# Kernel optimization log

Measured on AMD Instinct MI355X. Metric: run time of the kernel, lower is better.

Reference implementation:

```python
import jax, jax.numpy as jnp
import numpy as np
from jax import lax

B, F_BINS, T = 4, 196, 1000
DM, H, DEPTH, FFN, L, EDIM = 512, 8, 64, 2048, 4, 128


def setup_inputs() -> dict:
    key = jax.random.key(0)
    ks = jax.random.split(key, 16)
    d = {}
    d['spec'] = jax.random.normal(ks[0], (B, 1, F_BINS, T), jnp.float32)
    d['conv1_w'] = jax.random.normal(ks[1], (32, 1, 5, 5), jnp.float32) / 5.0
    d['conv1_b'] = jax.random.normal(ks[2], (32,), jnp.float32) * 0.01
    d['conv2_w'] = jax.random.normal(ks[3], (64, 32, 5, 5), jnp.float32) / np.sqrt(32 * 25)
    d['conv2_b'] = jax.random.normal(ks[4], (64,), jnp.float32) * 0.01
    d['proj_w'] = jax.random.normal(ks[5], (DM, 64), jnp.float32) / 8.0
    d['proj_b'] = jnp.zeros((DM,), jnp.float32)
    d['ln1_g'] = jnp.ones((L, DM), jnp.float32)
    d['ln1_b'] = jnp.zeros((L, DM), jnp.float32)
    s = 1.0 / np.sqrt(DM)
    for i, nm in enumerate(['qw', 'kw', 'vw', 'dw']):
        d[nm] = jax.random.normal(ks[6 + i], (L, DM, DM), jnp.float32) * s
    for nm in ['qb', 'kb', 'vb', 'db']:
        d[nm] = jnp.zeros((L, DM), jnp.float32)
    d['Er'] = jax.random.normal(ks[10], (L, T, DEPTH), jnp.float32)
    d['ln2_g'] = jnp.ones((L, DM), jnp.float32)
    d['ln2_b'] = jnp.zeros((L, DM), jnp.float32)
    d['f1w'] = jax.random.normal(ks[11], (L, FFN, DM), jnp.float32) * s
    d['f1b'] = jnp.zeros((L, FFN), jnp.float32)
    d['f2w'] = jax.random.normal(ks[12], (L, DM, FFN), jnp.float32) / np.sqrt(FFN)
    d['f2b'] = jnp.zeros((L, DM), jnp.float32)
    d['deproj_w'] = jax.random.normal(ks[13], (EDIM, DM), jnp.float32) * s
    d['deproj_b'] = jnp.zeros((EDIM,), jnp.float32)
    return d


def _layernorm(x, g, b, eps=1e-5):
    mu = jnp.mean(x, -1, keepdims=True)
    var = jnp.mean(jnp.square(x - mu), -1, keepdims=True)
    return g * (x - mu) / jnp.sqrt(var + eps) + b


def _skew(QEr):
    # QEr: [B,H,S,S] -> music-transformer skew trick
    b, h, s, _ = QEr.shape
    padded = jnp.pad(QEr, ((0, 0), (0, 0), (0, 0), (1, 0)))  # [B,H,S,S+1]
    return padded.reshape(b, h, s + 1, s)[:, :, 1:, :]


def _forward(spec, conv1_w, conv1_b, conv2_w, conv2_b, proj_w, proj_b,
             ln1_g, ln1_b, qw, qb, kw, kb, vw, vb, dw, db, Er,
             ln2_g, ln2_b, f1w, f1b, f2w, f2b, deproj_w, deproj_b):
    dn = ('NCHW', 'OIHW', 'NCHW')
    x = lax.conv_general_dilated(spec, conv1_w, (1, 1), 'SAME', dimension_numbers=dn)
    x = jax.nn.gelu(x + conv1_b[None, :, None, None], approximate=False)
    x = lax.reduce_window(x, -jnp.inf, lax.max, (1, 1, 14, 1), (1, 1, 14, 1), 'VALID')
    x = lax.conv_general_dilated(x, conv2_w, (1, 1), 'SAME', dimension_numbers=dn)
    x = jax.nn.gelu(x + conv2_b[None, :, None, None], approximate=False)
    x = lax.reduce_window(x, -jnp.inf, lax.max, (1, 1, 14, 1), (1, 1, 14, 1), 'VALID')
    x = x.reshape(B, 64, T)              # freq collapsed to 1, flatten(1,2)
    x = x.transpose(0, 2, 1)             # [B,T,64]
    x = x @ proj_w.T + proj_b            # [B,T,DM]
    scale = 1.0 / np.sqrt(DEPTH)
    for l in range(L):
        xn = _layernorm(x, ln1_g[l], ln1_b[l])
        Q = (xn @ qw[l].T + qb[l]).reshape(B, T, H, DEPTH).transpose(0, 2, 1, 3)
        K = (xn @ kw[l].T + kb[l]).reshape(B, T, H, DEPTH).transpose(0, 2, 1, 3)
        V = (xn @ vw[l].T + vb[l]).reshape(B, T, H, DEPTH).transpose(0, 2, 1, 3)
        QEr = jnp.einsum('bhsd,rd->bhsr', Q, Er[l])        # relative pos scores
        Srel = _skew(QEr)
        logits = (jnp.einsum('bhsd,bhtd->bhst', Q, K) + Srel) * scale
        attn = jax.nn.softmax(logits, axis=-1)
        out = jnp.einsum('bhst,bhtd->bhsd', attn, V)
        out = out.transpose(0, 2, 1, 3).reshape(B, T, DM)
        x = x + (out @ dw[l].T + db[l])
        xn2 = _layernorm(x, ln2_g[l], ln2_b[l])
        ff = jax.nn.relu(xn2 @ f1w[l].T + f1b[l]) @ f2w[l].T + f2b[l]
        x = x + ff
    return x @ deproj_w.T + deproj_b     # [B,T,EDIM]


def reference(spec, conv1_w, conv1_b, conv2_w, conv2_b, proj_w, proj_b,
              ln1_g, ln1_b, qw, qb, kw, kb, vw, vb, dw, db, Er,
              ln2_g, ln2_b, f1w, f1b, f2w, f2b, deproj_w, deproj_b):
    return _forward(spec, conv1_w, conv1_b, conv2_w, conv2_b, proj_w, proj_b,
                    ln1_g, ln1_b, qw, qb, kw, kb, vw, vb, dw, db, Er,
                    ln2_g, ln2_b, f1w, f1b, f2w, f2b, deproj_w, deproj_b)
```

## Files before the change

### kernel.cpp

```cpp
#include <hip/hip_runtime.h>
#include <hip/hip_bf16.h>
#include <hip/hip_fp16.h>
#include <math.h>

#define BB 4
#define FBINS 196
#define TT 1000
#define DM 512
#define HH 8
#define DEPTH 64
#define FFN 2048
#define LL 4
#define EDIM 128
#define BT (BB*TT)
#define PSHIFT 12.0f

typedef __hip_bfloat16 bf16;
typedef __attribute__((ext_vector_type(8))) short short8;
typedef __attribute__((ext_vector_type(4))) float floatx4;

#define ARENA_BYTES 420000000ULL
static void* g_arena = nullptr;
__attribute__((constructor)) static void arena_init() {
    if (!g_arena) (void)hipMalloc(&g_arena, ARENA_BYTES);
}

__device__ __forceinline__ float gelu_f(float x) {
    return 0.5f * x * (1.0f + erff(x * 0.70710678118654752440f));
}

__global__ __launch_bounds__(256) void sniff_k(const unsigned short* __restrict__ p,
                                               int n, int* __restrict__ cnt) {
    int i = blockIdx.x * 256 + threadIdx.x;
    int c = 0;
    for (; i < n; i += gridDim.x * 256) {
        unsigned short u = p[i];
        if ((unsigned short)(u & 0x7FFF) > (unsigned short)0x7F80) c++;
    }
    if (c) atomicAdd(cnt, c);
}

#define NCVT 17
struct CvtArgs {
    const void* src[NCVT];
    unsigned dst[NCVT];
    unsigned cum[NCVT + 1];
    const int* cnt;
    float* dstA;
};
__global__ __launch_bounds__(256) void cvt_all(CvtArgs a) {
    unsigned i = blockIdx.x * 256 + threadIdx.x;
    if (i >= a.cum[NCVT]) return;
    bool isb = (*a.cnt == 0);
    int w = 0;
    while (i >= a.cum[w + 1]) w++;
    unsigned j = i - a.cum[w];
    float v = isb ? __bfloat162float(((const bf16*)a.src[w])[j])
                  : ((const float*)a.src[w])[j];
    a.dstA[a.dst[w] + j] = v;
}

__global__ __launch_bounds__(256) void f2bf_dyn(const void* __restrict__ src,
                                                bf16* __restrict__ d, int n,
                                                const int* __restrict__ cnt) {
    int i = blockIdx.x * 256 + threadIdx.x;
    if (i >= n) return;
    if (*cnt == 0) d[i] = ((const bf16*)src)[i];
    else           d[i] = __float2bfloat16(((const float*)src)[i]);
}

__global__ __launch_bounds__(256) void w2perm(const void* __restrict__ src,
                                              bf16* __restrict__ d,
                                              const int* __restrict__ cnt) {
    int idx = blockIdx.x * 256 + threadIdx.x;
    if (idx >= 51200) return;
    int c = idx / 800, k = idx - c * 800;
    int kc = k >> 5, ci = k & 31;
    int di = kc / 5, dj = kc - di * 5;
    int s = ((c * 32 + ci) * 5 + di) * 5 + dj;
    float v = (*cnt == 0) ? __bfloat162float(((const bf16*)src)[s])
                          : ((const float*)src)[s];
    d[idx] = __float2bfloat16(v);
}

__global__ __launch_bounds__(256) void conv1_pool2(const float* __restrict__ spec,
                                                   const float* __restrict__ w1,
                                                   const float* __restrict__ b1,
                                                   bf16* __restrict__ P1c) {
    __shared__ float ss[18][256];
    __shared__ float sw[200];
    int jt = blockIdx.x, p = blockIdx.y, z = blockIdx.z;
    int b = z >> 2, cg = z & 3;
    int tid = threadIdx.x;
    for (int i = tid; i < 200; i += 256) sw[i] = w1[cg * 200 + i];
    int ibase = p * 14, c0 = jt * 250 - 2;
    for (int idx = tid; idx < 18 * 256; idx += 256) {
        int rr = idx >> 8, cc = idx & 255;
        int gi = ibase - 2 + rr, gj = c0 + cc;
        ss[rr][cc] = (gi >= 0 && gi < FBINS && gj >= 0 && gj < TT && cc < 254)
                         ? spec[(size_t)b * FBINS * TT + (size_t)gi * TT + gj] : 0.f;
    }
    __syncthreads();
    if (tid >= 250) return;
    int j = jt * 250 + tid;
    unsigned short* orow = (unsigned short*)P1c + ((size_t)((b * 14 + p) * 1000 + j)) * 32;
    for (int cpl = 0; cpl < 8; cpl += 2) {
        int cp = cg * 8 + cpl;
        float conv[2][14];
        float b0 = b1[cp], b1v = b1[cp + 1];
#pragma unroll
        for (int i = 0; i < 14; i++) { conv[0][i] = b0; conv[1][i] = b1v; }
        const float* w0 = sw + cpl * 25;
        const float* w1p = sw + (cpl + 1) * 25;
        for (int rr = 0; rr < 18; rr++) {
            float v0 = ss[rr][tid], v1 = ss[rr][tid + 1], v2 = ss[rr][tid + 2],
                  v3 = ss[rr][tid + 3], v4 = ss[rr][tid + 4];
#pragma unroll
            for (int di = 0; di < 5; di++) {
                int i = rr - di;
                if (i >= 0 && i < 14) {
                    conv[0][i] += v0 * w0[di * 5] + v1 * w0[di * 5 + 1] + v2 * w0[di * 5 + 2]
                                + v3 * w0[di * 5 + 3] + v4 * w0[di * 5 + 4];
                    conv[1][i] += v0 * w1p[di * 5] + v1 * w1p[di * 5 + 1] + v2 * w1p[di * 5 + 2]
                                + v3 * w1p[di * 5 + 3] + v4 * w1p[di * 5 + 4];
                }
            }
        }
        float mx0 = -1e30f, mn0 = 1e30f, mx1 = -1e30f, mn1 = 1e30f;
#pragma unroll
        for (int i = 0; i < 14; i++) {
            mx0 = fmaxf(mx0, conv[0][i]); mn0 = fminf(mn0, conv[0][i]);
            mx1 = fmaxf(mx1, conv[1][i]); mn1 = fminf(mn1, conv[1][i]);
        }
        float m0 = fmaxf(gelu_f(mx0), gelu_f(mn0));
        float m1 = fmaxf(gelu_f(mx1), gelu_f(mn1));
        bf16 mb0 = __float2bfloat16(m0), mb1 = __float2bfloat16(m1);
        unsigned pk = ((unsigned)(*(unsigned short*)&mb1) << 16) |
                      (unsigned)(*(unsigned short*)&mb0);
        *(unsigned*)(orow + cp) = pk;
    }
}

__global__ __launch_bounds__(256) void conv2_gemm(const bf16* __restrict__ P1c,
                                                  const bf16* __restrict__ W2p,
                                                  const float* __restrict__ c2b,
                                                  bf16* __restrict__ convout) {
    __shared__ __align__(16) short Asm[64 * 40];
    __shared__ __align__(16) short Bsm[64 * 40];
    int tid = threadIdx.x, wave = tid >> 6, lane = tid & 63;
    int q = lane >> 4, l15 = lane & 15;
    int jt = blockIdx.x, i = blockIdx.y, b = blockIdx.z;
    int lrow = tid >> 2, lci = (tid & 3) * 8;
    int jrow = jt * 64 + lrow;
    int mw = (wave & 1) * 32, nw = (wave >> 1) * 32;
    floatx4 acc[2][2] = {};
    for (int di = 0; di < 5; di++) {
        int ii = i + di - 2;
        bool iok = (ii >= 0 && ii < 14);
        for (int dj = 0; dj < 5; dj++) {
            int kc = di * 5 + dj;
            {
                int jj = jrow + dj - 2;
                uint4 v = make_uint4(0u, 0u, 0u, 0u);
                if (iok && jrow < TT && jj >= 0 && jj < TT)
                    v = *(const uint4*)(P1c +
                        (((size_t)(b * 14 + ii)) * TT + jj) * 32 + lci);
                *(uint4*)(Asm + lrow * 40 + lci) = v;
            }
            {
                *(uint4*)(Bsm + lrow * 40 + lci) =
                    *(const uint4*)(W2p + (size_t)lrow * 800 + kc * 32 + lci);
            }
            __syncthreads();
            short8 a0 = *(const short8*)(Asm + (mw + l15) * 40 + q * 8);
            short8 a1 = *(const short8*)(Asm + (mw + 16 + l15) * 40 + q * 8);
            short8 b0 = *(const short8*)(Bsm + (nw + l15) * 40 + q * 8);
            short8 b1 = *(const short8*)(Bsm + (nw + 16 + l15) * 40 + q * 8);
            acc[0][0] = __builtin_amdgcn_mfma_f32_16x16x32_bf16(a0, b0, acc[0][0], 0, 0, 0);
            acc[0][1] = __builtin_amdgcn_mfma_f32_16x16x32_bf16(a0, b1, acc[0][1], 0, 0, 0);
            acc[1][0] = __builtin_amdgcn_mfma_f32_16x16x32_bf16(a1, b0, acc[1][0], 0, 0, 0);
            acc[1][1] = __builtin_amdgcn_mfma_f32_16x16x32_bf16(a1, b1, acc[1][1], 0, 0, 0);
            __syncthreads();
        }
    }
#pragma unroll
    for (int im = 0; im < 2; im++) {
#pragma unroll
        for (int jn = 0; jn < 2; jn++) {
            int c = nw + jn * 16 + l15;
            float bv = c2b[c];
#pragma unroll
            for (int r = 0; r < 4; r++) {
                int j = jt * 64 + mw + im * 16 + q * 4 + r;
                if (j >= TT) continue;
                convout[((size_t)(b * 14 + i) * TT + j) * 64 + c] =
                    __float2bfloat16(acc[im][jn][r] + bv);
            }
        }
    }
}

__global__ __launch_bounds__(256) void pool2_k(const bf16* __restrict__ convout,
                                               bf16* __restrict__ p2t) {
    int idx = blockIdx.x * 256 + threadIdx.x;
    if (idx >= 256000) return;
    int c = idx & 63, bj = idx >> 6;
    int b = bj / 1000, j = bj - b * 1000;
    float mx = -1e30f, mn = 1e30f;
#pragma unroll
    for (int i = 0; i < 14; i++) {
        float v = __bfloat162float(convout[((size_t)(b * 14 + i) * 1000 + j) * 64 + c]);
        mx = fmaxf(mx, v); mn = fminf(mn, v);
    }
    p2t[(size_t)bj * 64 + c] = __float2bfloat16(fmaxf(gelu_f(mx), gelu_f(mn)));
}

__global__ __launch_bounds__(256) void layernorm_k(const float* __restrict__ x,
                                                   const float* __restrict__ g,
                                                   const float* __restrict__ bta,
                                                   bf16* __restrict__ y) {
    __shared__ float red[256];
    int row = blockIdx.x, tid = threadIdx.x;
    const float* xr = x + (size_t)row * DM;
    float v0 = xr[tid], v1 = xr[tid + 256];
    red[tid] = v0 + v1;
    __syncthreads();
    for (int s = 128; s > 0; s >>= 1) { if (tid < s) red[tid] += red[tid + s]; __syncthreads(); }
    float mu = red[0] * (1.f / 512.f);
    __syncthreads();
    float d0 = v0 - mu, d1 = v1 - mu;
    red[tid] = d0 * d0 + d1 * d1;
    __syncthreads();
    for (int s = 128; s > 0; s >>= 1) { if (tid < s) red[tid] += red[tid + s]; __syncthreads(); }
    float rstd = rsqrtf(red[0] * (1.f / 512.f) + 1e-5f);
    bf16* yr = y + (size_t)row * DM;
    yr[tid]       = __float2bfloat16(d0 * rstd * g[tid]       + bta[tid]);
    yr[tid + 256] = __float2bfloat16(d1 * rstd * g[tid + 256] + bta[tid + 256]);
}

__global__ __launch_bounds__(256) void gemm_out(const float* __restrict__ A,
                                                const float* __restrict__ B,
                                                const float* __restrict__ bias,
                                                const int* __restrict__ cnt,
                                                void* __restrict__ dout,
                                                int M, int N, int K) {
    __shared__ float As[32][33];
    __shared__ float Bs[32][33];
    int tid = threadIdx.x;
    int tx = tid & 15, ty = tid >> 4;
    int m0 = blockIdx.x * 32, n0 = blockIdx.y * 32;
    float c[2][2] = {};
    for (int k0 = 0; k0 < K; k0 += 32) {
#pragma unroll
        for (int i = 0; i < 4; i++) {
            int idx = i * 256 + tid;
            int r = idx >> 5, kk = idx & 31;
            int gm = m0 + r;
            As[r][kk] = (gm < M) ? A[(size_t)gm * K + k0 + kk] : 0.f;
            Bs[r][kk] = B[(size_t)(n0 + r) * K + k0 + kk];
        }
        __syncthreads();
#pragma unroll
        for (int k = 0; k < 32; k++) {
            float a0 = As[ty * 2][k], a1 = As[ty * 2 + 1][k];
            float b0 = Bs[tx * 2][k], b1 = Bs[tx * 2 + 1][k];
            c[0][0] += a0 * b0; c[0][1] += a0 * b1;
            c[1][0] += a1 * b0; c[1][1] += a1 * b1;
        }
        __syncthreads();
    }
    bool isb = (*cnt == 0);
#pragma unroll
    for (int i = 0; i < 2; i++) {
        int m = m0 + ty * 2 + i;
        if (m >= M) continue;
#pragma unroll
        for (int jj = 0; jj < 2; jj++) {
            int n = n0 + tx * 2 + jj;
            float v = c[i][jj] + bias[n];
            if (isb) ((bf16*)dout)[(size_t)m * N + n] = __float2bfloat16(v);
            else     ((float*)dout)[(size_t)m * N + n] = v;
        }
    }
}

template <int BM, int NT, int ROUTE, int ACT, bool OUT_BF16>
__global__ __launch_bounds__(256) void mfma_big(const bf16* __restrict__ A,
                                                const bf16* __restrict__ B,
                                                const float* __restrict__ bias,
                                                const float* __restrict__ resid,
                                                float* __restrict__ Cf,
                                                bf16* __restrict__ Cb,
                                                int M, int N, int K,
                                                size_t wstride, int bstride,
                                                size_t ostride) {
    __shared__ __align__(16) short Asm[BM * 40];
    __shared__ __align__(16) short Bsm[NT * 40];
    int tid = threadIdx.x, wave = tid >> 6, lane = tid & 63;
    int q = lane >> 4, l15 = lane & 15;
    int m0 = blockIdx.x * BM, n0 = blockIdx.y * NT;
    int lrow = tid >> 2, lk = (tid & 3) * 8;
    constexpr int MF = (NT == 128) ? (BM / 16) : (BM / 32);
    int m0w = (NT == 128) ? 0 : ((wave >> 1) * (BM / 2));
    int nfb = (NT == 128) ? (wave * 32) : ((wave & 1) * 32);
    floatx4 acc[MF][2] = {};
    for (int k0 = 0; k0 < K; k0 += 32) {
#pragma unroll
        for (int hh = 0; hh < BM / 64; hh++) {
            int row = lrow + hh * 64, gm = m0 + row;
            uint4 v = make_uint4(0u, 0u, 0u, 0u);
            if (gm < M) v = *(const uint4*)(A + (size_t)gm * K + k0 + lk);
            *(uint4*)(Asm + row * 40 + lk) = v;
        }
#pragma unroll
        for (int hh = 0; hh < NT / 64; hh++) {
            int row = lrow + hh * 64, gn = n0 + row;
            const bf16* src = ROUTE
                ? B + (size_t)(gn >> 9) * wstride + (size_t)(gn & 511) * K + k0 + lk
                : B + (size_t)gn * K + k0 + lk;
            *(uint4*)(Bsm + row * 40 + lk) = *(const uint4*)src;
        }
        __syncthreads();
        short8 a[MF], b2[2];
#pragma unroll
        for (int im = 0; im < MF; im++)
            a[im] = *(const short8*)(Asm + (m0w + im * 16 + l15) * 40 + q * 8);
#pragma unroll
        for (int jn = 0; jn < 2; jn++)
            b2[jn] = *(const short8*)(Bsm + (nfb + jn * 16 + l15) * 40 + q * 8);
#pragma unroll
        for (int im = 0; im < MF; im++)
#pragma unroll
            for (int jn = 0; jn < 2; jn++)
                acc[im][jn] = __builtin_amdgcn_mfma_f32_16x16x32_bf16(
                    a[im], b2[jn], acc[im][jn], 0, 0, 0);
        __syncthreads();
    }
#pragma unroll
    for (int im = 0; im < MF; im++) {
#pragma unroll
        for (int jn = 0; jn < 2; jn++) {
            int nn = n0 + nfb + jn * 16 + l15;
            float bval = ROUTE ? bias[(nn >> 9) * bstride + (nn & 511)] : bias[nn];
#pragma unroll
            for (int r = 0; r < 4; r++) {
                int m = m0 + m0w + im * 16 + q * 4 + r;
                if (m >= M) continue;
                float v = acc[im][jn][r] + bval;
                if (resid) v += resid[(size_t)m * N + nn];
                if (ACT == 1) v = fmaxf(v, 0.f);
                if (ROUTE)
                    Cb[(size_t)(nn >> 9) * ostride + (size_t)m * 512 + (nn & 511)] =
                        __float2bfloat16(v);
                else if (OUT_BF16)
                    Cb[(size_t)m * N + nn] = __float2bfloat16(v);
                else
                    Cf[(size_t)m * N + nn] = v;
            }
        }
    }
}

__global__ __launch_bounds__(256) void vt_k(const bf16* __restrict__ Vb,
                                            bf16* __restrict__ Vt) {
    __shared__ short tile[64][65];
    int t0 = blockIdx.x * 64, z = blockIdx.y;
    int b = z >> 3, h = z & 7;
    int tid = threadIdx.x;
#pragma unroll
    for (int i = 0; i < 16; i++) {
        int tr = i * 4 + (tid >> 6), d = tid & 63;
        int t = t0 + tr;
        bf16 v = (t < TT) ? Vb[((size_t)b * TT + t) * DM + h * 64 + d] : (bf16)__float2bfloat16(0.f);
        tile[tr][d] = *(short*)&v;
    }
    __syncthreads();
#pragma unroll
    for (int i = 0; i < 16; i++) {
        int dr = i * 4 + (tid >> 6), tc = tid & 63;
        *(short*)&Vt[(size_t)z * 65536 + dr * 1024 + t0 + tc] = tile[tc][dr];
    }
}

__global__ __launch_bounds__(256, 2) void attn_fused(const bf16* __restrict__ Q,
                                                     const bf16* __restrict__ K,
                                                     const bf16* __restrict__ Er,
                                                     const bf16* __restrict__ Vt,
                                                     bf16* __restrict__ AO) {
    __shared__ __align__(16) short Qs[6400];
    __shared__ __align__(16) short pool[13000];
    __shared__ __align__(16) short Pl[64 * 136];
    __shared__ __align__(16) short Vs[64 * 136];
    __shared__ float rsw[4][64];
    int tid = threadIdx.x, wave = tid >> 6, lane = tid & 63;
    int q = lane >> 4, l15 = lane & 15;
    int m0 = blockIdx.x * 64;
    int z = blockIdx.z, b = z >> 3, h = z & 7;
    const bf16* Ap = Q + (size_t)b * TT * DM + h * 64;
    const bf16* Bp = K + (size_t)b * TT * DM + h * 64;
    const bf16* Vp = Vt + (size_t)z * 65536;
    int lrow = tid >> 2, lk = (tid & 3) * 8;
    int mw = wave * 16;

#pragma unroll
    for (int kh = 0; kh < 2; kh++) {
        int gm = m0 + lrow;
        uint4 v = make_uint4(0u, 0u, 0u, 0u);
        if (gm < TT) v = *(const uint4*)(Ap + (size_t)gm * DM + kh * 32 + lk);
        *(uint4*)(Qs + kh * 3200 + lrow * 40 + lk) = v;
        if (tid < 64) {
            int rr = 64 + (tid >> 2);
            int g2 = m0 + rr;
            uint4 v2 = make_uint4(0u, 0u, 0u, 0u);
            if (g2 < TT) v2 = *(const uint4*)(Ap + (size_t)g2 * DM + kh * 32 + lk);
            *(uint4*)(Qs + kh * 3200 + rr * 40 + lk) = v2;
        }
    }

    float rsum[16];
#pragma unroll
    for (int i = 0; i < 16; i++) rsum[i] = 0.f;
    floatx4 accO[4] = {};

    for (int tc = 0; tc < 8; tc++) {
        int t0 = tc * 128;
        int db = t0 - m0 - 64;
        floatx4 accS[4][2] = {};
        floatx4 accG[5][3] = {};
        for (int k0 = 0; k0 < 64; k0 += 32) {
            {
                int gn = t0 + lrow;
                uint4 v0 = make_uint4(0u, 0u, 0u, 0u), v1 = v0;
                if (gn < TT)      v0 = *(const uint4*)(Bp + (size_t)gn * DM + k0 + lk);
                if (gn + 64 < TT) v1 = *(const uint4*)(Bp + (size_t)(gn + 64) * DM + k0 + lk);
                *(uint4*)(pool + lrow * 40 + lk) = v0;
                *(uint4*)(pool + (lrow + 64) * 40 + lk) = v1;
            }
            {
#pragma unroll
                for (int hh = 0; hh < 3; hh++) {
                    int dd = lrow + hh * 64;
                    int dl = db + dd;
                    int src = (dl <= 0) ? (999 + dl) : (dl - 1);
                    uint4 v = make_uint4(0u, 0u, 0u, 0u);
                    if (src >= 0 && src < TT)
                        v = *(const uint4*)(Er + (size_t)src * 64 + k0 + lk);
                    *(uint4*)(pool + 5120 + dd * 40 + lk) = v;
                }
            }
            if (k0 == 0) {
#pragma unroll
                for (int e = 0; e < 4; e++) {
                    int li = tid + e * 256;
                    int row = li >> 4, cs = (li & 15) * 8;
                    *(uint4*)(Vs + row * 136 + cs) =
                        *(const uint4*)(Vp + (size_t)row * 1024 + t0 + cs);
                }
            }
            __syncthreads();
            short8 a[5], bk[2], e[3];
#pragma unroll
            for (int im = 0; im < 5; im++)
                a[im] = *(const short8*)(Qs + (k0 >> 5) * 3200 + (im * 16 + l15) * 40 + q * 8);
#pragma unroll
            for (int jn = 0; jn < 2; jn++)
                bk[jn] = *(const short8*)(pool + (wave * 32 + jn * 16 + l15) * 40 + q * 8);
#pragma unroll
            for (int jg = 0; jg < 3; jg++)
                e[jg] = *(const short8*)(pool + 5120 + (wave * 48 + jg * 16 + l15) * 40 + q * 8);
#pragma unroll
            for (int im = 0; im < 4; im++)
#pragma unroll
                for (int jn = 0; jn < 2; jn++)
                    accS[im][jn] = __builtin_amdgcn_mfma_f32_16x16x32_bf16(
                        a[im], bk[jn], accS[im][jn], 0, 0, 0);
#pragma unroll
            for (int im = 0; im < 5; im++)
#pragma unroll
                for (int jg = 0; jg < 3; jg++)
                    accG[im][jg] = __builtin_amdgcn_mfma_f32_16x16x32_bf16(
                        a[im], e[jg], accG[im][jg], 0, 0, 0);
            __syncthreads();
        }
#pragma unroll
        for (int im = 0; im < 5; im++)
#pragma unroll
            for (int jg = 0; jg < 3; jg++) {
                int col = wave * 48 + jg * 16 + l15;
#pragma unroll
                for (int r = 0; r < 4; r++) {
                    int row = im * 16 + q * 4 + r;
                    if (row < 65) {
                        bf16 gv = __float2bfloat16(accG[im][jg][r]);
                        pool[row * 200 + col] = *(short*)&gv;
                    }
                }
            }
        __syncthreads();
#pragma unroll
        for (int im = 0; im < 4; im++)
#pragma unroll
            for (int jn = 0; jn < 2; jn++) {
                int nl = wave * 32 + jn * 16 + l15;
                int n = t0 + nl;
#pragma unroll
                for (int r = 0; r < 4; r++) {
                    int ml = im * 16 + q * 4 + r;
                    int m = m0 + ml;
                    float pe = 0.f;
                    if (n < TT) {
                        float rel = 0.f;
                        if (n != m + 1) {
                            int u = (n <= m) ? m : (m + 1);
                            int dd = n - u - db;
                            short gs = pool[(u - m0) * 200 + dd];
                            rel = __bfloat162float(*(bf16*)&gs);
                        }
                        pe = __expf((accS[im][jn][r] + rel) * 0.125f - PSHIFT);
                        rsum[im * 4 + r] += pe;
                    }
                    bf16 pb = __float2bfloat16(pe);
                    Pl[ml * 136 + nl] = *(short*)&pb;
                }
            }
        __syncthreads();
#pragma unroll
        for (int kc = 0; kc < 4; kc++) {
            short8 a = *(const short8*)(Pl + (mw + l15) * 136 + kc * 32 + q * 8);
#pragma unroll
            for (int jn = 0; jn < 4; jn++) {
                short8 bv = *(const short8*)(Vs + (jn * 16 + l15) * 136 + kc * 32 + q * 8);
                accO[jn] = __builtin_amdgcn_mfma_f32_16x16x32_bf16(a, bv, accO[jn], 0, 0, 0);
            }
        }
        __syncthreads();
    }
#pragma unroll
    for (int t = 0; t < 16; t++) {
        float s = rsum[t];
        s += __shfl_xor(s, 1, 64); s += __shfl_xor(s, 2, 64);
        s += __shfl_xor(s, 4, 64); s += __shfl_xor(s, 8, 64);
        if (l15 == 0) rsw[wave][(t >> 2) * 16 + q * 4 + (t & 3)] = s;
    }
    __syncthreads();
#pragma unroll
    for (int r = 0; r < 4; r++) {
        int lm = mw + q * 4 + r;
        int m = m0 + lm;
        if (m >= TT) continue;
        float inv = 1.f / (rsw[0][lm] + rsw[1][lm] + rsw[2][lm] + rsw[3][lm]);
#pragma unroll
        for (int jn = 0; jn < 4; jn++)
            AO[((size_t)b * TT + m) * DM + h * 64 + jn * 16 + l15] =
                __float2bfloat16(accO[jn][r] * inv);
    }
}

extern "C" void kernel_launch(void* const* d_in, const int* in_sizes, int n_in,
                              void* d_out, int out_size, void* d_ws, size_t ws_size,
                              hipStream_t stream) {
    if (!g_arena) (void)hipMalloc(&g_arena, ARENA_BYTES);
    float* A = (float*)g_arena;

    static const unsigned off[27] = {
        0, 784000, 784800, 784832, 836032, 836096, 868864, 869376, 871424,
        873472, 1922048, 2970624, 4019200, 5067776, 5069824, 5071872,
        5073920, 5075968, 5331968, 5334016, 5336064, 9530368, 9538560,
        13732864, 13734912, 13800448, 13800576};
    const float* spec  = A + off[0];
    const float* c1w   = A + off[1];
    const float* c1b   = A + off[2];
    const float* c2b   = A + off[4];
    const float* projb = A + off[6];
    const float* ln1g  = A + off[7];
    const float* ln1b  = A + off[8];
    const float* qb    = A + off[13];
    const float* db    = A + off[16];
    const float* ln2g  = A + off[18];
    const float* ln2b  = A + off[19];
    const float* f1b   = A + off[21];
    const float* f2b_  = A + off[23];
    const float* depw  = A + off[24];
    const float* depb  = A + off[25];

    const size_t PA = 13800576;
    float* x    = A + PA;
    float* P1   = x + 2048000;
    float* SM   = P1 + 1792000;
    bf16* P1c     = (bf16*)P1;
    bf16* p2t_b   = (bf16*)SM;
    bf16* projw_b = (bf16*)(SM + 128000);
    bf16* w2p     = (bf16*)(SM + 150000);
    int*   cnt  = (int*)(SM + 256000);
    float* ScF  = SM + 256004;
    float* B0   = ScF + 32000000;
    bf16* wb_qkvd = (bf16*)B0;
    bf16* wb_f1   = (bf16*)(B0 + 2097152);
    bf16* wb_f2   = (bf16*)(B0 + 4194304);
    bf16* Erb     = (bf16*)(B0 + 6291456);
    bf16* xn_b    = (bf16*)(B0 + 6419456);
    bf16* AO_b    = (bf16*)(B0 + 7443456);
    bf16* Qb_b    = (bf16*)(B0 + 8467456);
    bf16* Kb_b    = (bf16*)(B0 + 9491456);
    bf16* Vb_b    = (bf16*)(B0 + 10515456);
    bf16* FFH_b   = (bf16*)(B0 + 11539456);
    bf16* Vt      = (bf16*)(B0 + 15635456);
    bf16* convout = (bf16*)(B0 + 16684032);

    hipMemsetAsync(cnt, 0, sizeof(int), stream);
    sniff_k<<<1024, 256, 0, stream>>>((const unsigned short*)d_in[20], 1000000, cnt);

    static const int cvt_ids[NCVT] = {0, 1, 2, 4, 6, 7, 8, 13, 14, 15, 16,
                                      18, 19, 21, 23, 24, 25};
    CvtArgs ca;
    unsigned cum = 0;
    for (int t = 0; t < NCVT; t++) {
        int w = cvt_ids[t];
        ca.src[t] = d_in[w];
        ca.dst[t] = off[w];
        ca.cum[t] = cum;
        cum += off[w + 1] - off[w];
    }
    ca.cum[NCVT] = cum;
    ca.cnt = cnt; ca.dstA = A;
    cvt_all<<<(cum + 255) / 256, 256, 0, stream>>>(ca);

    for (int t = 0; t < 4; t++)
        f2bf_dyn<<<4096, 256, 0, stream>>>(d_in[9 + t], wb_qkvd + (size_t)t * 1048576,
                                           1048576, cnt);
    f2bf_dyn<<<16384, 256, 0, stream>>>(d_in[20], wb_f1, 4194304, cnt);
    f2bf_dyn<<<16384, 256, 0, stream>>>(d_in[22], wb_f2, 4194304, cnt);
    f2bf_dyn<<<1000,  256, 0, stream>>>(d_in[17], Erb,   256000, cnt);
    f2bf_dyn<<<128,   256, 0, stream>>>(d_in[5],  projw_b, 32768, cnt);
    w2perm<<<200, 256, 0, stream>>>(d_in[3], w2p, cnt);

    conv1_pool2<<<dim3(4, 14, 16), 256, 0, stream>>>(spec, c1w, c1b, P1c);
    conv2_gemm<<<dim3(16, 14, 4), 256, 0, stream>>>(P1c, w2p, c2b, convout);
    pool2_k<<<1000, 256, 0, stream>>>(convout, p2t_b);
    mfma_big<64, 64, 0, 0, false><<<dim3(63, 8), 256, 0, stream>>>(
        p2t_b, projw_b, projb, nullptr, x, nullptr, BT, DM, 64, 0, 0, 0);

    for (int l = 0; l < LL; l++) {
        layernorm_k<<<BT, 256, 0, stream>>>(x, ln1g + l * DM, ln1b + l * DM, xn_b);
        mfma_big<128, 128, 1, 0, true><<<dim3(32, 12), 256, 0, stream>>>(
            xn_b, wb_qkvd + (size_t)l * DM * DM, qb + l * DM, nullptr,
            nullptr, Qb_b, BT, 1536, DM, 1048576, 2048, 2048000);
        vt_k<<<dim3(16, 32), 256, 0, stream>>>(Vb_b, Vt);
        attn_fused<<<dim3(16, 1, 32), 256, 0, stream>>>(
            Qb_b, Kb_b, Erb + (size_t)l * TT * DEPTH, Vt, AO_b);
        mfma_big<64, 64, 0, 0, false><<<dim3(63, 8), 256, 0, stream>>>(
            AO_b, wb_qkvd + 3 * 1048576 + (size_t)l * DM * DM, db + l * DM, x,
            x, nullptr, BT, DM, DM, 0, 0, 0);
        layernorm_k<<<BT, 256, 0, stream>>>(x, ln2g + l * DM, ln2b + l * DM, xn_b);
        mfma_big<128, 128, 0, 1, true><<<dim3(32, 16), 256, 0, stream>>>(
            xn_b, wb_f1 + (size_t)l * FFN * DM, f1b + l * FFN, nullptr,
            nullptr, FFH_b, BT, FFN, DM, 0, 0, 0);
        mfma_big<64, 64, 0, 0, false><<<dim3(63, 8), 256, 0, stream>>>(
            FFH_b, wb_f2 + (size_t)l * DM * FFN, f2b_ + l * DM, x,
            x, nullptr, BT, DM, FFN, 0, 0, 0);
    }

    gemm_out<<<dim3(125, 4), 256, 0, stream>>>(x, depw, depb, cnt, d_out, BT, EDIM, DM);
}
```

Before: 1.089 ms.

## Transpose QK^T MFMA and scatter skewed relative scores directly into P tile

The QK^T product is computed as K·Q^T so that each lane holds four consecutive key columns for one query row. The relative-position scores are written already skewed into the Pl tile, replacing the intermediate pool buffer and its per-element gather. The softmax pass then reads and writes Pl with packed 64-bit accesses, and the row-sum reduction shrinks from 16 to 4 partial sums per lane. This aims to cut LDS traffic, index arithmetic and shuffle work in the attention kernel, at the cost of a more intricate skew-scatter indexing that must handle the diagonal zero case correctly.

```diff
diff --git a/kernel.cpp b/kernel.cpp
--- a/kernel.cpp
+++ b/kernel.cpp
@@ -388,7 +388,7 @@
                                                      const bf16* __restrict__ Vt,
                                                      bf16* __restrict__ AO) {
     __shared__ __align__(16) short Qs[6400];
-    __shared__ __align__(16) short pool[13000];
+    __shared__ __align__(16) short pool[12800];
     __shared__ __align__(16) short Pl[64 * 136];
     __shared__ __align__(16) short Vs[64 * 136];
     __shared__ float rsw[4][64];
@@ -417,15 +417,13 @@
         }
     }
 
-    float rsum[16];
-#pragma unroll
-    for (int i = 0; i < 16; i++) rsum[i] = 0.f;
+    float rsum[4] = {0.f, 0.f, 0.f, 0.f};
     floatx4 accO[4] = {};
 
     for (int tc = 0; tc < 8; tc++) {
         int t0 = tc * 128;
         int db = t0 - m0 - 64;
-        floatx4 accS[4][2] = {};
+        floatx4 accS[2][4] = {};
         floatx4 accG[5][3] = {};
         for (int k0 = 0; k0 < 64; k0 += 32) {
             {
@@ -458,71 +456,81 @@
                 }
             }
             __syncthreads();
-            short8 a[5], bk[2], e[3];
+            short8 qf[5], kf[2], e[3];
 #pragma unroll
             for (int im = 0; im < 5; im++)
-                a[im] = *(const short8*)(Qs + (k0 >> 5) * 3200 + (im * 16 + l15) * 40 + q * 8);
-#pragma unroll
-            for (int jn = 0; jn < 2; jn++)
-                bk[jn] = *(const short8*)(pool + (wave * 32 + jn * 16 + l15) * 40 + q * 8);
+                qf[im] = *(const short8*)(Qs + (k0 >> 5) * 3200 + (im * 16 + l15) * 40 + q * 8);
+#pragma unroll
+            for (int i = 0; i < 2; i++)
+                kf[i] = *(const short8*)(pool + ((2 * wave + i) * 16 + l15) * 40 + q * 8);
 #pragma unroll
             for (int jg = 0; jg < 3; jg++)
                 e[jg] = *(const short8*)(pool + 5120 + (wave * 48 + jg * 16 + l15) * 40 + q * 8);
 #pragma unroll
-            for (int im = 0; im < 4; im++)
-#pragma unroll
-                for (int jn = 0; jn < 2; jn++)
-                    accS[im][jn] = __builtin_amdgcn_mfma_f32_16x16x32_bf16(
-                        a[im], bk[jn], accS[im][jn], 0, 0, 0);
+            for (int i = 0; i < 2; i++)
+#pragma unroll
+                for (int j = 0; j < 4; j++)
+                    accS[i][j] = __builtin_amdgcn_mfma_f32_16x16x32_bf16(
+                        kf[i], qf[j], accS[i][j], 0, 0, 0);
 #pragma unroll
             for (int im = 0; im < 5; im++)
 #pragma unroll
                 for (int jg = 0; jg < 3; jg++)
                     accG[im][jg] = __builtin_amdgcn_mfma_f32_16x16x32_bf16(
-                        a[im], e[jg], accG[im][jg], 0, 0, 0);
+                        qf[im], e[jg], accG[im][jg], 0, 0, 0);
             __syncthreads();
         }
 #pragma unroll
-        for (int im = 0; im < 5; im++)
-#pragma unroll
-            for (int jg = 0; jg < 3; jg++) {
-                int col = wave * 48 + jg * 16 + l15;
+        for (int jg = 0; jg < 3; jg++) {
+            int dd = wave * 48 + jg * 16 + l15;
+            int delta = dd + db;
+            int nlb = dd - 64;
+#pragma unroll
+            for (int im = 0; im < 5; im++) {
 #pragma unroll
                 for (int r = 0; r < 4; r++) {
-                    int row = im * 16 + q * 4 + r;
-                    if (row < 65) {
-                        bf16 gv = __float2bfloat16(accG[im][jg][r]);
-                        pool[row * 200 + col] = *(short*)&gv;
+                    int ur = im * 16 + q * 4 + r;
+                    int nl = ur + nlb;
+                    if (nl >= 0 && nl < 128) {
+                        int mr = (delta <= 0) ? ur : (ur - 1);
+                        if (mr >= 0 && mr < 64) {
+                            bf16 gb = __float2bfloat16(accG[im][jg][r]);
+                            Pl[mr * 136 + nl] = *(short*)&gb;
+                        }
+                        if (delta == 0 && ur >= 1 && ur <= 64)
+                            Pl[(ur - 1) * 136 + nl] = 0;
                     }
                 }
             }
+        }
         __syncthreads();
 #pragma unroll
-        for (int im = 0; im < 4; im++)
-#pragma unroll
-            for (int jn = 0; jn < 2; jn++) {
-                int nl = wave * 32 + jn * 16 + l15;
-                int n = t0 + nl;
+        for (int i = 0; i < 2; i++) {
+            int nt = (2 * wave + i) * 16 + q * 4;
+#pragma unroll
+            for (int j = 0; j < 4; j++) {
+                int ml = j * 16 + l15;
+                uint2 rq = *(const uint2*)(Pl + ml * 136 + nt);
+                unsigned short rh[4] = {
+                    (unsigned short)(rq.x & 0xFFFF), (unsigned short)(rq.x >> 16),
+                    (unsigned short)(rq.y & 0xFFFF), (unsigned short)(rq.y >> 16)};
+                unsigned short o4[4];
 #pragma unroll
                 for (int r = 0; r < 4; r++) {
-                    int ml = im * 16 + q * 4 + r;
-                    int m = m0 + ml;
-                    float pe = 0.f;
-                    if (n < TT) {
-                        float rel = 0.f;
-                        if (n != m + 1) {
-                            int u = (n <= m) ? m : (m + 1);
-                            int dd = n - u - db;
-                            short gs = pool[(u - m0) * 200 + dd];
-                            rel = __bfloat162float(*(bf16*)&gs);
-                        }
-                        pe = __expf((accS[im][jn][r] + rel) * 0.125f - PSHIFT);
-                        rsum[im * 4 + r] += pe;
-                    }
-                    bf16 pb = __float2bfloat16(pe);
-                    Pl[ml * 136 + nl] = *(short*)&pb;
+                    int n = t0 + nt + r;
+                    float rel = __bfloat162float(*(bf16*)&rh[r]);
+                    float pv = __expf((accS[i][j][r] + rel) * 0.125f - PSHIFT);
+                    pv = (n < TT) ? pv : 0.f;
+                    rsum[j] += pv;
+                    bf16 pb = __float2bfloat16(pv);
+                    o4[r] = *(unsigned short*)&pb;
                 }
-            }
+                uint2 w;
+                w.x = (unsigned)o4[0] | ((unsigned)o4[1] << 16);
+                w.y = (unsigned)o4[2] | ((unsigned)o4[3] << 16);
+                *(uint2*)(Pl + ml * 136 + nt) = w;
+            }
+        }
         __syncthreads();
 #pragma unroll
         for (int kc = 0; kc < 4; kc++) {
@@ -536,11 +544,11 @@
         __syncthreads();
     }
 #pragma unroll
-    for (int t = 0; t < 16; t++) {
-        float s = rsum[t];
-        s += __shfl_xor(s, 1, 64); s += __shfl_xor(s, 2, 64);
-        s += __shfl_xor(s, 4, 64); s += __shfl_xor(s, 8, 64);
-        if (l15 == 0) rsw[wave][(t >> 2) * 16 + q * 4 + (t & 3)] = s;
+    for (int j = 0; j < 4; j++) {
+        float s = rsum[j];
+        s += __shfl_xor(s, 16, 64);
+        s += __shfl_xor(s, 32, 64);
+        if (q == 0) rsw[wave][j * 16 + l15] = s;
     }
     __syncthreads();
 #pragma unroll
```

New measurement: 1.211 ms. 1.11x slower.
